# Kernel tuning notes

Measured on AMD Instinct MI355X. Metric: run time of the kernel, lower is better.

## Reference

```python
import jax, jax.numpy as jnp
import numpy as np

NUM_CLASSES = 1000
DENSE_DIM = 64 * 64  # 4096, hardcoded in the module
BATCH = 8192
W0, W1 = 0.5, 0.5  # self.weights


def setup_inputs() -> dict:
    key = jax.random.key(0)
    k1, k2, k3, k4 = jax.random.split(key, 4)
    logits = jax.random.normal(k1, (BATCH, NUM_CLASSES), dtype=jnp.float32)
    dense_out = jax.random.normal(k2, (BATCH, DENSE_DIM), dtype=jnp.float32)
    target = jax.random.randint(k3, (BATCH,), 0, NUM_CLASSES, dtype=jnp.int32)
    # dense_labels buffer: random 0/1 per (class, dense) cell, as in __init__
    dense_labels = jax.random.bernoulli(k4, 0.5, (NUM_CLASSES, DENSE_DIM)).astype(jnp.float32)
    return {"logits": logits, "dense_out": dense_out, "target": target,
            "dense_labels": dense_labels}


def _bce_with_logits_mean(x, y):
    # numerically stable BCEWithLogitsLoss (mean reduction)
    return jnp.mean(jnp.maximum(x, 0.0) - x * y + jnp.log1p(jnp.exp(-jnp.abs(x))))


def reference(logits, dense_out, target, dense_labels):
    # --- accumulation (detached in the original; side-effect state) ---
    probs = jax.lax.stop_gradient(jax.nn.sigmoid(dense_out))  # [B, D]
    dense_output_sum = jax.ops.segment_sum(probs, target, num_segments=NUM_CLASSES)  # [C, D]
    total_accumulated = jax.ops.segment_sum(
        jnp.ones((BATCH,), dtype=jnp.float32), target, num_segments=NUM_CLASSES)  # [C]

    # --- losses ---
    dense_target = dense_labels[target]  # per-sample gather of label rows [B, D]
    logp = jax.nn.log_softmax(logits, axis=-1)
    loss1 = -jnp.mean(jnp.take_along_axis(logp, target[:, None], axis=1))  # CrossEntropyLoss
    loss2 = _bce_with_logits_mean(dense_out, dense_target)
    loss = loss1 * W0 + loss2 * W1
    return loss, dense_output_sum, total_accumulated
```

## Files before the change

kernel.cpp:

```cpp
#include <hip/hip_runtime.h>
#include <math.h>

#define NC   1000
#define DD   4096
#define BB   8192

#define MAIN_BLOCKS (NC * 4)
#define CE_BLOCKS   (BB / 4)
#define TOT_BLOCKS  (MAIN_BLOCKS + CE_BLOCKS)
#define MAXN 128
#define NSLOT 32


#define ACC1(xv, yv, acc)                                                     \
    {                                                                         \
        float e = __expf(-fabsf(xv));                                         \
        float inv = __builtin_amdgcn_rcpf(1.f + e);                           \
        acc += (xv >= 0.f) ? inv : e * inv;                                   \
        bce += fmaxf(xv, 0.f) - xv * yv + __logf(1.f + e);                    \
    }

__global__ __launch_bounds__(256) void fused_k(const float* __restrict__ logits,
                                               const float* __restrict__ dense_out,
                                               const int*   __restrict__ target,
                                               const float* __restrict__ dense_labels,
                                               float* __restrict__ out,
                                               double* __restrict__ loss1,
                                               double* __restrict__ loss2) {
    int bx = blockIdx.x;
    int t  = threadIdx.x;
    int wave = t >> 6;
    int lane = t & 63;

    __shared__ int   sidx[MAXN];
    __shared__ int   s_n;
    __shared__ float red[4];

    if (bx < MAIN_BLOCKS) {
        int c     = bx >> 2;
        int chunk = bx & 3;
        int d     = chunk * 1024 + (t << 2);

        if (t == 0) s_n = 0;
        __syncthreads();

        const int4* tp = (const int4*)target;
        #pragma unroll
        for (int k = 0; k < 8; ++k) {
            int4 v = tp[k * 256 + t];
            int s0 = (k * 256 + t) * 4;
            if (v.x == c) { int p = atomicAdd(&s_n, 1); sidx[p] = s0;     }
            if (v.y == c) { int p = atomicAdd(&s_n, 1); sidx[p] = s0 + 1; }
            if (v.z == c) { int p = atomicAdd(&s_n, 1); sidx[p] = s0 + 2; }
            if (v.w == c) { int p = atomicAdd(&s_n, 1); sidx[p] = s0 + 3; }
        }
        __syncthreads();
        int n = s_n;

        float4 y = *(const float4*)(dense_labels + (size_t)c * DD + d);
        float a0 = 0.f, a1 = 0.f, a2 = 0.f, a3 = 0.f, bce = 0.f;
        const float* dp = dense_out + d;

        for (int base = 0; base < n; base += 8) {
            int m = n - base; if (m > 8) m = 8;
            float4 xb[8];
            #pragma unroll
            for (int j = 0; j < 8; ++j)
                if (j < m) xb[j] = *(const float4*)(dp + (size_t)sidx[base + j] * DD);
            #pragma unroll
            for (int j = 0; j < 8; ++j)
                if (j < m) {
                    ACC1(xb[j].x, y.x, a0) ACC1(xb[j].y, y.y, a1)
                    ACC1(xb[j].z, y.z, a2) ACC1(xb[j].w, y.w, a3)
                }
        }

        float* p = out + 1 + (size_t)c * DD + d;
        p[0] = a0; p[1] = a1; p[2] = a2; p[3] = a3;

        if (chunk == 0 && t == 0) out[1 + (size_t)NC * DD + c] = (float)n;

        #pragma unroll
        for (int o2 = 32; o2 > 0; o2 >>= 1) bce += __shfl_xor(bce, o2);
        if (lane == 0) red[wave] = bce;
        __syncthreads();
        if (t == 0)
            atomicAdd(&loss2[bx & (NSLOT - 1)],
                      (double)(red[0] + red[1] + red[2] + red[3]));
    } else {
        int i = (bx - MAIN_BLOCKS) * 4 + wave;
        const float* row = logits + (size_t)i * NC;
        int j0 = lane * 4;

        float4 r0 = *(const float4*)(row + j0);
        float4 r1 = *(const float4*)(row + j0 + 256);
        float4 r2 = *(const float4*)(row + j0 + 512);
        float4 r3;
        if (j0 + 768 < NC) r3 = *(const float4*)(row + j0 + 768);
        else r3 = make_float4(-INFINITY, -INFINITY, -INFINITY, -INFINITY);
        float tl = row[target[i]];

        float mx = fmaxf(fmaxf(fmaxf(r0.x, r0.y), fmaxf(r0.z, r0.w)),
                         fmaxf(fmaxf(r1.x, r1.y), fmaxf(r1.z, r1.w)));
        mx = fmaxf(mx, fmaxf(fmaxf(r2.x, r2.y), fmaxf(r2.z, r2.w)));
        mx = fmaxf(mx, fmaxf(fmaxf(r3.x, r3.y), fmaxf(r3.z, r3.w)));
        #pragma unroll
        for (int o = 32; o > 0; o >>= 1) mx = fmaxf(mx, __shfl_xor(mx, o));

        float s = __expf(r0.x - mx) + __expf(r0.y - mx) + __expf(r0.z - mx) + __expf(r0.w - mx)
                + __expf(r1.x - mx) + __expf(r1.y - mx) + __expf(r1.z - mx) + __expf(r1.w - mx)
                + __expf(r2.x - mx) + __expf(r2.y - mx) + __expf(r2.z - mx) + __expf(r2.w - mx)
                + __expf(r3.x - mx) + __expf(r3.y - mx) + __expf(r3.z - mx) + __expf(r3.w - mx);
        #pragma unroll
        for (int o = 32; o > 0; o >>= 1) s += __shfl_xor(s, o);

        if (lane == 0) red[wave] = -(tl - mx - __logf(s));
        __syncthreads();
        if (t == 0)
            atomicAdd(&loss1[bx & (NSLOT - 1)],
                      (double)(red[0] + red[1] + red[2] + red[3]));
    }
}

__global__ void fin_k(const double* __restrict__ loss1,
                      const double* __restrict__ loss2,
                      float* __restrict__ out) {
    double l1 = 0.0, l2 = 0.0;
    #pragma unroll
    for (int i = 0; i < NSLOT; ++i) { l1 += loss1[i]; l2 += loss2[i]; }
    out[0] = (float)(0.5 * (l1 / (double)BB) +
                     0.5 * (l2 / ((double)BB * (double)DD)));
}

extern "C" void kernel_launch(void* const* d_in, const int* in_sizes, int n_in,
                              void* d_out, int out_size, void* d_ws, size_t ws_size,
                              hipStream_t stream) {
    const float* logits       = (const float*)d_in[0];
    const float* dense_out    = (const float*)d_in[1];
    const int*   target       = (const int*)d_in[2];
    const float* dense_labels = (const float*)d_in[3];
    float* out = (float*)d_out;

    char* ws = (char*)d_ws;
    double* loss1 = (double*)(ws + 0);
    double* loss2 = (double*)(ws + 256);

    hipMemsetAsync(d_ws, 0, 512, stream);

    fused_k<<<TOT_BLOCKS, 256, 0, stream>>>(logits, dense_out, target,
                                            dense_labels, out, loss1, loss2);
    fin_k<<<1, 1, 0, stream>>>(loss1, loss2, out);
}
```

Measured before the change: 251.5 us.

## Build CSR bucket of samples per class instead of per-block target scans

Replaces the per-block full scan of the 8192-entry target array (done by all 4000 main blocks) with a count, prefix-scan and scatter sequence of kernels that builds a CSR list of sample indices per class. The main kernel then reads its class's index range directly, loads indices unconditionally with clamping so the eight row loads can be issued without branching, and drops the shared-memory block reduction in favour of per-wave atomics. Cross-entropy moves to its own kernel. This adds several small launches and serialization between them, and the sample order within a class becomes nondeterministic, which changes the float summation order of the outputs.

```diff
diff --git a/kernel.cpp b/kernel.cpp
--- a/kernel.cpp
+++ b/kernel.cpp
@@ -4,13 +4,77 @@
 #define NC   1000
 #define DD   4096
 #define BB   8192
-
-#define MAIN_BLOCKS (NC * 4)
-#define CE_BLOCKS   (BB / 4)
-#define TOT_BLOCKS  (MAIN_BLOCKS + CE_BLOCKS)
-#define MAXN 128
 #define NSLOT 32
 
+
+__global__ void count_k(const int* __restrict__ target, int* __restrict__ counts) {
+    int i = blockIdx.x * blockDim.x + threadIdx.x;
+    atomicAdd(&counts[target[i]], 1);
+}
+
+__global__ __launch_bounds__(1024) void scan_k(const int* __restrict__ counts,
+                                               int* __restrict__ offsets) {
+    __shared__ int sh[1024];
+    int t = threadIdx.x;
+    int orig = (t < NC) ? counts[t] : 0;
+    sh[t] = orig;
+    __syncthreads();
+    for (int off = 1; off < 1024; off <<= 1) {
+        int v = (t >= off) ? sh[t - off] : 0;
+        __syncthreads();
+        sh[t] += v;
+        __syncthreads();
+    }
+    offsets[t] = sh[t] - orig;
+}
+
+__global__ void scatter_k(const int* __restrict__ target,
+                          const int* __restrict__ offsets,
+                          int* __restrict__ cursor, int* __restrict__ csr) {
+    int i = blockIdx.x * blockDim.x + threadIdx.x;
+    int t = target[i];
+    int pos = offsets[t] + atomicAdd(&cursor[t], 1);
+    csr[pos] = i;
+}
+
+__global__ __launch_bounds__(256) void ce_k(const float* __restrict__ logits,
+                                            const int* __restrict__ target,
+                                            double* __restrict__ loss1) {
+    int wave = threadIdx.x >> 6;
+    int lane = threadIdx.x & 63;
+    int i = blockIdx.x * 4 + wave;
+    const float* row = logits + (size_t)i * NC;
+    int j0 = lane * 4;
+
+    float4 r0 = *(const float4*)(row + j0);
+    float4 r1 = *(const float4*)(row + j0 + 256);
+    float4 r2 = *(const float4*)(row + j0 + 512);
+    float4 r3;
+    if (j0 + 768 < NC) r3 = *(const float4*)(row + j0 + 768);
+    else r3 = make_float4(-INFINITY, -INFINITY, -INFINITY, -INFINITY);
+    float tl = row[target[i]];
+
+    float mx = fmaxf(fmaxf(fmaxf(r0.x, r0.y), fmaxf(r0.z, r0.w)),
+                     fmaxf(fmaxf(r1.x, r1.y), fmaxf(r1.z, r1.w)));
+    mx = fmaxf(mx, fmaxf(fmaxf(r2.x, r2.y), fmaxf(r2.z, r2.w)));
+    mx = fmaxf(mx, fmaxf(fmaxf(r3.x, r3.y), fmaxf(r3.z, r3.w)));
+    #pragma unroll
+    for (int o = 32; o > 0; o >>= 1) mx = fmaxf(mx, __shfl_xor(mx, o));
+
+    float s = __expf(r0.x - mx) + __expf(r0.y - mx) + __expf(r0.z - mx) + __expf(r0.w - mx)
+            + __expf(r1.x - mx) + __expf(r1.y - mx) + __expf(r1.z - mx) + __expf(r1.w - mx)
+            + __expf(r2.x - mx) + __expf(r2.y - mx) + __expf(r2.z - mx) + __expf(r2.w - mx)
+            + __expf(r3.x - mx) + __expf(r3.y - mx) + __expf(r3.z - mx) + __expf(r3.w - mx);
+    #pragma unroll
+    for (int o = 32; o > 0; o >>= 1) s += __shfl_xor(s, o);
+
+    __shared__ float red[4];
+    if (lane == 0) red[wave] = -(tl - mx - __logf(s));
+    __syncthreads();
+    if (threadIdx.x == 0)
+        atomicAdd(&loss1[blockIdx.x & (NSLOT - 1)],
+                  (double)(red[0] + red[1] + red[2] + red[3]));
+}
 
 #define ACC1(xv, yv, acc)                                                     \
     {                                                                         \
@@ -20,106 +84,54 @@
         bce += fmaxf(xv, 0.f) - xv * yv + __logf(1.f + e);                    \
     }
 
-__global__ __launch_bounds__(256) void fused_k(const float* __restrict__ logits,
-                                               const float* __restrict__ dense_out,
-                                               const int*   __restrict__ target,
-                                               const float* __restrict__ dense_labels,
-                                               float* __restrict__ out,
-                                               double* __restrict__ loss1,
-                                               double* __restrict__ loss2) {
-    int bx = blockIdx.x;
-    int t  = threadIdx.x;
-    int wave = t >> 6;
-    int lane = t & 63;
+__global__ __launch_bounds__(256) void main_k(const float* __restrict__ dense_out,
+                                              const float* __restrict__ dense_labels,
+                                              const int* __restrict__ counts,
+                                              const int* __restrict__ offsets,
+                                              const int* __restrict__ csr,
+                                              float* __restrict__ out,
+                                              double* __restrict__ loss2) {
+    int c     = blockIdx.x;
+    int chunk = blockIdx.y;
+    int t     = threadIdx.x;
+    int d     = chunk * 1024 + (t << 2);
+    int n = counts[c];
+    int o = offsets[c];
 
-    __shared__ int   sidx[MAXN];
-    __shared__ int   s_n;
-    __shared__ float red[4];
+    float4 y = *(const float4*)(dense_labels + (size_t)c * DD + d);
+    float a0 = 0.f, a1 = 0.f, a2 = 0.f, a3 = 0.f, bce = 0.f;
+    const float* dp = dense_out + d;
 
-    if (bx < MAIN_BLOCKS) {
-        int c     = bx >> 2;
-        int chunk = bx & 3;
-        int d     = chunk * 1024 + (t << 2);
+    for (int base = 0; base < n; base += 8) {
+        int idx[8];
+        #pragma unroll
+        for (int j = 0; j < 8; ++j) {
+            int s = base + j;
+            s = (s < n) ? s : (n - 1);
+            idx[j] = csr[o + s];
+        }
+        float4 xb[8];
+        #pragma unroll
+        for (int j = 0; j < 8; ++j)
+            xb[j] = *(const float4*)(dp + (size_t)idx[j] * DD);
+        #pragma unroll
+        for (int j = 0; j < 8; ++j) {
+            if (base + j < n) {
+                ACC1(xb[j].x, y.x, a0) ACC1(xb[j].y, y.y, a1)
+                ACC1(xb[j].z, y.z, a2) ACC1(xb[j].w, y.w, a3)
+            }
+        }
+    }
 
-        if (t == 0) s_n = 0;
-        __syncthreads();
+    float* p = out + 1 + (size_t)c * DD + d;
+    p[0] = a0; p[1] = a1; p[2] = a2; p[3] = a3;
 
-        const int4* tp = (const int4*)target;
-        #pragma unroll
-        for (int k = 0; k < 8; ++k) {
-            int4 v = tp[k * 256 + t];
-            int s0 = (k * 256 + t) * 4;
-            if (v.x == c) { int p = atomicAdd(&s_n, 1); sidx[p] = s0;     }
-            if (v.y == c) { int p = atomicAdd(&s_n, 1); sidx[p] = s0 + 1; }
-            if (v.z == c) { int p = atomicAdd(&s_n, 1); sidx[p] = s0 + 2; }
-            if (v.w == c) { int p = atomicAdd(&s_n, 1); sidx[p] = s0 + 3; }
-        }
-        __syncthreads();
-        int n = s_n;
+    if (chunk == 0 && t == 0) out[1 + (size_t)NC * DD + c] = (float)n;
 
-        float4 y = *(const float4*)(dense_labels + (size_t)c * DD + d);
-        float a0 = 0.f, a1 = 0.f, a2 = 0.f, a3 = 0.f, bce = 0.f;
-        const float* dp = dense_out + d;
-
-        for (int base = 0; base < n; base += 8) {
-            int m = n - base; if (m > 8) m = 8;
-            float4 xb[8];
-            #pragma unroll
-            for (int j = 0; j < 8; ++j)
-                if (j < m) xb[j] = *(const float4*)(dp + (size_t)sidx[base + j] * DD);
-            #pragma unroll
-            for (int j = 0; j < 8; ++j)
-                if (j < m) {
-                    ACC1(xb[j].x, y.x, a0) ACC1(xb[j].y, y.y, a1)
-                    ACC1(xb[j].z, y.z, a2) ACC1(xb[j].w, y.w, a3)
-                }
-        }
-
-        float* p = out + 1 + (size_t)c * DD + d;
-        p[0] = a0; p[1] = a1; p[2] = a2; p[3] = a3;
-
-        if (chunk == 0 && t == 0) out[1 + (size_t)NC * DD + c] = (float)n;
-
-        #pragma unroll
-        for (int o2 = 32; o2 > 0; o2 >>= 1) bce += __shfl_xor(bce, o2);
-        if (lane == 0) red[wave] = bce;
-        __syncthreads();
-        if (t == 0)
-            atomicAdd(&loss2[bx & (NSLOT - 1)],
-                      (double)(red[0] + red[1] + red[2] + red[3]));
-    } else {
-        int i = (bx - MAIN_BLOCKS) * 4 + wave;
-        const float* row = logits + (size_t)i * NC;
-        int j0 = lane * 4;
-
-        float4 r0 = *(const float4*)(row + j0);
-        float4 r1 = *(const float4*)(row + j0 + 256);
-        float4 r2 = *(const float4*)(row + j0 + 512);
-        float4 r3;
-        if (j0 + 768 < NC) r3 = *(const float4*)(row + j0 + 768);
-        else r3 = make_float4(-INFINITY, -INFINITY, -INFINITY, -INFINITY);
-        float tl = row[target[i]];
-
-        float mx = fmaxf(fmaxf(fmaxf(r0.x, r0.y), fmaxf(r0.z, r0.w)),
-                         fmaxf(fmaxf(r1.x, r1.y), fmaxf(r1.z, r1.w)));
-        mx = fmaxf(mx, fmaxf(fmaxf(r2.x, r2.y), fmaxf(r2.z, r2.w)));
-        mx = fmaxf(mx, fmaxf(fmaxf(r3.x, r3.y), fmaxf(r3.z, r3.w)));
-        #pragma unroll
-        for (int o = 32; o > 0; o >>= 1) mx = fmaxf(mx, __shfl_xor(mx, o));
-
-        float s = __expf(r0.x - mx) + __expf(r0.y - mx) + __expf(r0.z - mx) + __expf(r0.w - mx)
-                + __expf(r1.x - mx) + __expf(r1.y - mx) + __expf(r1.z - mx) + __expf(r1.w - mx)
-                + __expf(r2.x - mx) + __expf(r2.y - mx) + __expf(r2.z - mx) + __expf(r2.w - mx)
-                + __expf(r3.x - mx) + __expf(r3.y - mx) + __expf(r3.z - mx) + __expf(r3.w - mx);
-        #pragma unroll
-        for (int o = 32; o > 0; o >>= 1) s += __shfl_xor(s, o);
-
-        if (lane == 0) red[wave] = -(tl - mx - __logf(s));
-        __syncthreads();
-        if (t == 0)
-            atomicAdd(&loss1[bx & (NSLOT - 1)],
-                      (double)(red[0] + red[1] + red[2] + red[3]));
-    }
+    #pragma unroll
+    for (int o2 = 32; o2 > 0; o2 >>= 1) bce += __shfl_xor(bce, o2);
+    if ((t & 63) == 0)
+        atomicAdd(&loss2[(blockIdx.x * 4 + (t >> 6)) & (NSLOT - 1)], (double)bce);
 }
 
 __global__ void fin_k(const double* __restrict__ loss1,
@@ -142,12 +154,22 @@
     float* out = (float*)d_out;
 
     char* ws = (char*)d_ws;
-    double* loss1 = (double*)(ws + 0);
-    double* loss2 = (double*)(ws + 256);
+    double* loss1   = (double*)(ws + 0);
+    double* loss2   = (double*)(ws + 256);
+    int*    counts  = (int*)(ws + 512);
+    int*    cursor  = (int*)(ws + 4608);
+    int*    offsets = (int*)(ws + 8704);
+    int*    csr     = (int*)(ws + 12800);
 
-    hipMemsetAsync(d_ws, 0, 512, stream);
+    hipMemsetAsync(d_ws, 0, 8704, stream);
 
-    fused_k<<<TOT_BLOCKS, 256, 0, stream>>>(logits, dense_out, target,
-                                            dense_labels, out, loss1, loss2);
+    count_k<<<BB / 256, 256, 0, stream>>>(target, counts);
+    scan_k<<<1, 1024, 0, stream>>>(counts, offsets);
+    scatter_k<<<BB / 256, 256, 0, stream>>>(target, offsets, cursor, csr);
+    ce_k<<<BB / 4, 256, 0, stream>>>(logits, target, loss1);
+
+    dim3 grid(NC, 4);
+    main_k<<<grid, 256, 0, stream>>>(dense_out, dense_labels, counts, offsets, csr,
+                                     out, loss2);
     fin_k<<<1, 1, 0, stream>>>(loss1, loss2, out);
 }
```

New measurement: 318.8 us. 1.27x slower.

## Precompute per-class CSR index lists in a separate kernel instead of per-block scans

Applied to the files above, without the earlier changes.

Adds a single-block build kernel that histograms the targets, prefix-sums them and scatters sample indices into a CSR layout. Each main block then reads its class's index list directly instead of every block rescanning all 8192 targets with shared atomics. Blocks grow to 512 threads covering half a row, the gather loop loads all eight rows unconditionally using readfirstlane indices with a sched barrier, and the cross-wave reduction changes. The cost is an extra serialized single-block launch, and sidx is still capped at 128 entries per class.

```diff
diff --git a/kernel.cpp b/kernel.cpp
--- a/kernel.cpp
+++ b/kernel.cpp
@@ -4,13 +4,48 @@
 #define NC   1000
 #define DD   4096
 #define BB   8192
+#define NSLOT 32
+#define MAXN 128
 
-#define MAIN_BLOCKS (NC * 4)
-#define CE_BLOCKS   (BB / 4)
+#define MAIN_BLOCKS (NC * 2)
+#define CE_BLOCKS   (BB / 8)
 #define TOT_BLOCKS  (MAIN_BLOCKS + CE_BLOCKS)
-#define MAXN 128
-#define NSLOT 32
 
+
+__global__ __launch_bounds__(1024) void build_k(const int* __restrict__ target,
+                                                int* __restrict__ counts_g,
+                                                int* __restrict__ offsets_g,
+                                                int* __restrict__ csr) {
+    __shared__ int scnt[1024];
+    __shared__ int scur[1024];
+    int t = threadIdx.x;
+    scnt[t] = 0;
+    __syncthreads();
+    int tg[8];
+    #pragma unroll
+    for (int k = 0; k < 8; ++k) {
+        tg[k] = target[k * 1024 + t];
+        atomicAdd(&scnt[tg[k]], 1);
+    }
+    __syncthreads();
+    int orig = scnt[t];
+    __syncthreads();
+    for (int off = 1; off < 1024; off <<= 1) {
+        int v = (t >= off) ? scnt[t - off] : 0;
+        __syncthreads();
+        scnt[t] += v;
+        __syncthreads();
+    }
+    int excl = scnt[t] - orig;
+    if (t < NC) { counts_g[t] = orig; offsets_g[t] = excl; }
+    scur[t] = excl;
+    __syncthreads();
+    #pragma unroll
+    for (int k = 0; k < 8; ++k) {
+        int pos = atomicAdd(&scur[tg[k]], 1);
+        csr[pos] = k * 1024 + t;
+    }
+}
 
 #define ACC1(xv, yv, acc)                                                     \
     {                                                                         \
@@ -20,75 +55,74 @@
         bce += fmaxf(xv, 0.f) - xv * yv + __logf(1.f + e);                    \
     }
 
-__global__ __launch_bounds__(256) void fused_k(const float* __restrict__ logits,
-                                               const float* __restrict__ dense_out,
-                                               const int*   __restrict__ target,
-                                               const float* __restrict__ dense_labels,
-                                               float* __restrict__ out,
-                                               double* __restrict__ loss1,
-                                               double* __restrict__ loss2) {
+__global__ __launch_bounds__(512, 8) void fused_k(const float* __restrict__ logits,
+                                                  const float* __restrict__ dense_out,
+                                                  const int*   __restrict__ target,
+                                                  const float* __restrict__ dense_labels,
+                                                  const int*   __restrict__ counts,
+                                                  const int*   __restrict__ offsets,
+                                                  const int*   __restrict__ csr,
+                                                  float* __restrict__ out,
+                                                  double* __restrict__ loss1,
+                                                  double* __restrict__ loss2) {
     int bx = blockIdx.x;
     int t  = threadIdx.x;
     int wave = t >> 6;
     int lane = t & 63;
 
     __shared__ int   sidx[MAXN];
-    __shared__ int   s_n;
-    __shared__ float red[4];
+    __shared__ float red[8];
 
     if (bx < MAIN_BLOCKS) {
-        int c     = bx >> 2;
-        int chunk = bx & 3;
-        int d     = chunk * 1024 + (t << 2);
+        int c    = bx >> 1;
+        int half = bx & 1;
+        int d    = half * 2048 + (t << 2);
+        int n = counts[c];
+        int o = offsets[c];
 
-        if (t == 0) s_n = 0;
+        if (t < n && t < MAXN) sidx[t] = csr[o + t];
         __syncthreads();
-
-        const int4* tp = (const int4*)target;
-        #pragma unroll
-        for (int k = 0; k < 8; ++k) {
-            int4 v = tp[k * 256 + t];
-            int s0 = (k * 256 + t) * 4;
-            if (v.x == c) { int p = atomicAdd(&s_n, 1); sidx[p] = s0;     }
-            if (v.y == c) { int p = atomicAdd(&s_n, 1); sidx[p] = s0 + 1; }
-            if (v.z == c) { int p = atomicAdd(&s_n, 1); sidx[p] = s0 + 2; }
-            if (v.w == c) { int p = atomicAdd(&s_n, 1); sidx[p] = s0 + 3; }
-        }
-        __syncthreads();
-        int n = s_n;
 
         float4 y = *(const float4*)(dense_labels + (size_t)c * DD + d);
         float a0 = 0.f, a1 = 0.f, a2 = 0.f, a3 = 0.f, bce = 0.f;
         const float* dp = dense_out + d;
 
         for (int base = 0; base < n; base += 8) {
-            int m = n - base; if (m > 8) m = 8;
             float4 xb[8];
             #pragma unroll
-            for (int j = 0; j < 8; ++j)
-                if (j < m) xb[j] = *(const float4*)(dp + (size_t)sidx[base + j] * DD);
+            for (int j = 0; j < 8; ++j) {
+                int s = base + j;
+                s = (s < n) ? s : (n - 1);
+                int id = __builtin_amdgcn_readfirstlane(sidx[s]);
+                xb[j] = *(const float4*)(dp + (size_t)id * DD);
+            }
+            __builtin_amdgcn_sched_barrier(0);
             #pragma unroll
-            for (int j = 0; j < 8; ++j)
-                if (j < m) {
+            for (int j = 0; j < 8; ++j) {
+                if (base + j < n) {
                     ACC1(xb[j].x, y.x, a0) ACC1(xb[j].y, y.y, a1)
                     ACC1(xb[j].z, y.z, a2) ACC1(xb[j].w, y.w, a3)
                 }
+            }
         }
 
         float* p = out + 1 + (size_t)c * DD + d;
         p[0] = a0; p[1] = a1; p[2] = a2; p[3] = a3;
-
-        if (chunk == 0 && t == 0) out[1 + (size_t)NC * DD + c] = (float)n;
+        if (half == 0 && t == 0) out[1 + (size_t)NC * DD + c] = (float)n;
 
         #pragma unroll
         for (int o2 = 32; o2 > 0; o2 >>= 1) bce += __shfl_xor(bce, o2);
         if (lane == 0) red[wave] = bce;
         __syncthreads();
-        if (t == 0)
-            atomicAdd(&loss2[bx & (NSLOT - 1)],
-                      (double)(red[0] + red[1] + red[2] + red[3]));
+        if (wave == 0) {
+            float v = (lane < 8) ? red[lane] : 0.f;
+            #pragma unroll
+            for (int o2 = 4; o2 > 0; o2 >>= 1) v += __shfl_xor(v, o2);
+            if (lane == 0)
+                atomicAdd(&loss2[bx & (NSLOT - 1)], (double)v);
+        }
     } else {
-        int i = (bx - MAIN_BLOCKS) * 4 + wave;
+        int i = (bx - MAIN_BLOCKS) * 8 + wave;
         const float* row = logits + (size_t)i * NC;
         int j0 = lane * 4;
 
@@ -116,9 +150,13 @@
 
         if (lane == 0) red[wave] = -(tl - mx - __logf(s));
         __syncthreads();
-        if (t == 0)
-            atomicAdd(&loss1[bx & (NSLOT - 1)],
-                      (double)(red[0] + red[1] + red[2] + red[3]));
+        if (wave == 0) {
+            float v = (lane < 8) ? red[lane] : 0.f;
+            #pragma unroll
+            for (int o2 = 4; o2 > 0; o2 >>= 1) v += __shfl_xor(v, o2);
+            if (lane == 0)
+                atomicAdd(&loss1[bx & (NSLOT - 1)], (double)v);
+        }
     }
 }
 
@@ -142,12 +180,16 @@
     float* out = (float*)d_out;
 
     char* ws = (char*)d_ws;
-    double* loss1 = (double*)(ws + 0);
-    double* loss2 = (double*)(ws + 256);
+    double* loss1   = (double*)(ws + 0);
+    double* loss2   = (double*)(ws + 256);
+    int*    counts  = (int*)(ws + 512);
+    int*    offsets = (int*)(ws + 4608);
+    int*    csr     = (int*)(ws + 8704);
 
     hipMemsetAsync(d_ws, 0, 512, stream);
 
-    fused_k<<<TOT_BLOCKS, 256, 0, stream>>>(logits, dense_out, target,
-                                            dense_labels, out, loss1, loss2);
+    build_k<<<1, 1024, 0, stream>>>(target, counts, offsets, csr);
+    fused_k<<<TOT_BLOCKS, 512, 0, stream>>>(logits, dense_out, target, dense_labels,
+                                            counts, offsets, csr, out, loss1, loss2);
     fin_k<<<1, 1, 0, stream>>>(loss1, loss2, out);
 }
```

Measured after the change: 254.5 us. No clear change (+1.2%).
